# Performance work log

Measured on AMD Instinct MI355X. Metric: run time of the kernel, lower is better.

Reference implementation:

```python
import jax, jax.numpy as jnp
import numpy as np

B, S, H, NH = 2, 2048, 1024, 16
HD = H // NH  # head dim = 64


def setup_inputs() -> dict:
    key = jax.random.key(0)
    ks = jax.random.split(key, 11)
    s = 1.0 / np.sqrt(H)
    return {
        "q": jax.random.normal(ks[0], (B, S, H), jnp.float32),
        "k": jax.random.normal(ks[1], (B, S, H), jnp.float32),
        "v": jax.random.normal(ks[2], (B, S, H), jnp.float32),
        "Wq": jax.random.normal(ks[3], (H, H), jnp.float32) * s,
        "bq": jax.random.normal(ks[4], (H,), jnp.float32) * 0.02,
        "Wk": jax.random.normal(ks[5], (H, H), jnp.float32) * s,
        "bk": jax.random.normal(ks[6], (H,), jnp.float32) * 0.02,
        "Wv": jax.random.normal(ks[7], (H, H), jnp.float32) * s,
        "bv": jax.random.normal(ks[8], (H,), jnp.float32) * 0.02,
        "Wo": jax.random.normal(ks[9], (H, H), jnp.float32) * s,
        "bo": jax.random.normal(ks[10], (H,), jnp.float32) * 0.02,
    }


def reference(q, k, v, Wq, bq, Wk, bk, Wv, bv, Wo, bo):
    # QKV projections: [B,S,H]
    qp = q @ Wq + bq
    kp = k @ Wk + bk
    vp = v @ Wv + bv
    # split heads -> [B, NH, S, HD]
    def split(x):
        return x.reshape(B, S, NH, HD).transpose(0, 2, 1, 3)
    qh, kh, vh = split(qp), split(kp), split(vp)
    # scores [B, NH, S, S], scale by sqrt(head_dim)
    scores = jnp.einsum('bhqd,bhkd->bhqk', qh, kh) / jnp.sqrt(jnp.asarray(HD, qh.dtype))
    attn = jax.nn.softmax(scores, axis=-1)  # attention_dropout p=0.0 (eval)
    ctx = jnp.einsum('bhqk,bhkd->bhqd', attn, vh)
    # merge heads -> [B, S, H]
    ctx = ctx.transpose(0, 2, 1, 3).reshape(B, S, H)
    out = ctx @ Wo + bo  # dropout p=0.0 (eval)
    return out
```

## Files before the change

kernel.cpp:

```cpp
#include <hip/hip_runtime.h>

typedef unsigned short u16;
typedef __attribute__((ext_vector_type(8))) short bf16x8;
typedef __attribute__((ext_vector_type(4))) float f32x4;
typedef __attribute__((ext_vector_type(4))) unsigned short u16x4;

#define B_  2
#define S_  2048
#define H_  1024
#define NH_ 16
#define HD_ 64
#define MR_ (B_*S_)
#define K_  H_

__device__ __forceinline__ u16 f2bf(float f) {
  union { float f; unsigned u; } x; x.f = f;
  unsigned r = x.u + 0x7fffu + ((x.u >> 16) & 1u);
  return (u16)(r >> 16);
}

__device__ __forceinline__ unsigned cvtpk(float lo, float hi) {
  unsigned r;
  asm("v_cvt_pk_bf16_f32 %0, %1, %2" : "=v"(r) : "v"(lo), "v"(hi));
  return r;
}

__device__ __forceinline__ void gload16(const u16* g, u16* l) {
  __builtin_amdgcn_global_load_lds((const __attribute__((address_space(1))) void*)g,
                                   (__attribute__((address_space(3))) void*)l, 16, 0, 0);
}

__global__ __launch_bounds__(256) void cvt3(const float* __restrict__ q, const float* __restrict__ k,
                                            const float* __restrict__ v, u16* __restrict__ dst) {
  const float* src = blockIdx.z == 0 ? q : blockIdx.z == 1 ? k : v;
  u16* d = dst + (size_t)blockIdx.z * MR_ * H_;
  size_t i = ((size_t)blockIdx.x * 256 + threadIdx.x) * 4;
  float4 f = *(const float4*)(src + i);
  u16x4 o = { f2bf(f.x), f2bf(f.y), f2bf(f.z), f2bf(f.w) };
  *(u16x4*)(d + i) = o;
}

__global__ __launch_bounds__(256) void wtrans(const float* __restrict__ Wq, const float* __restrict__ Wk,
                                              const float* __restrict__ Wv, const float* __restrict__ Wo,
                                              u16* __restrict__ wt) {
  const int z = blockIdx.z;
  const float* W = z == 0 ? Wq : z == 1 ? Wk : z == 2 ? Wv : Wo;
  u16* Wt = wt + (size_t)z * H_ * K_;
  __shared__ float t[32][33];
  const int n0 = blockIdx.x * 32, k0 = blockIdx.y * 32;
  const int tx = threadIdx.x & 31, ty = threadIdx.x >> 5;
  #pragma unroll
  for (int i = 0; i < 4; i++) t[ty + 8*i][tx] = W[(size_t)(k0 + ty + 8*i) * H_ + n0 + tx];
  __syncthreads();
  #pragma unroll
  for (int i = 0; i < 4; i++) Wt[(size_t)(n0 + ty + 8*i) * K_ + k0 + tx] = f2bf(t[tx][ty + 8*i]);
}

template <int MODE>
__device__ __forceinline__ void gemm_body(const u16* __restrict__ A, const u16* __restrict__ Bt,
                                          const float* __restrict__ bias, float scale,
                                          u16* __restrict__ Obf, float* __restrict__ Of,
                                          int m_tile, int n_tile) {
  __shared__ u16 ldsA[128 * 64];
  __shared__ u16 ldsB[128 * 64];
  const int tid = threadIdx.x;
  const int lane = tid & 63, wave = tid >> 6;
  const int wm = wave >> 1, wn = wave & 1;
  const int m0 = m_tile * 128, n0 = n_tile * 128;

  f32x4 acc[4][4] = {};

  const int srow = tid >> 3;
  const int sslot = (tid & 7) ^ (srow & 7);
  const u16* ga = A + (size_t)(m0 + srow) * K_ + sslot * 8;
  const u16* gb = Bt + (size_t)(n0 + srow) * K_ + sslot * 8;
  u16* la = ldsA + tid * 8;
  u16* lb = ldsB + tid * 8;

  const int fr = lane & 15;
  const int kg = lane >> 4;

  for (int k0 = 0; k0 < K_; k0 += 64) {
    #pragma unroll
    for (int j = 0; j < 4; j++) gload16(ga + (size_t)(j * 32) * K_ + k0, la + j * 2048);
    #pragma unroll
    for (int j = 0; j < 4; j++) gload16(gb + (size_t)(j * 32) * K_ + k0, lb + j * 2048);
    __syncthreads();

    #pragma unroll
    for (int kk = 0; kk < 2; kk++) {
      const int ps = (((kk << 2) | kg) ^ (fr & 7)) * 8;
      bf16x8 a[4], b[4];
      #pragma unroll
      for (int mf = 0; mf < 4; mf++)
        a[mf] = *(const bf16x8*)&ldsA[(wm * 64 + mf * 16 + fr) * 64 + ps];
      #pragma unroll
      for (int nf = 0; nf < 4; nf++)
        b[nf] = *(const bf16x8*)&ldsB[(wn * 64 + nf * 16 + fr) * 64 + ps];
      #pragma unroll
      for (int mf = 0; mf < 4; mf++)
        #pragma unroll
        for (int nf = 0; nf < 4; nf++)
          acc[mf][nf] = __builtin_amdgcn_mfma_f32_16x16x32_bf16(a[mf], b[nf], acc[mf][nf], 0, 0, 0);
    }
    __syncthreads();
  }

  float bcol[4];
  #pragma unroll
  for (int nf = 0; nf < 4; nf++) bcol[nf] = bias[n0 + wn * 64 + nf * 16 + fr];

  if (MODE == 2) {
    #pragma unroll
    for (int mf = 0; mf < 4; mf++) {
      const int row0 = m0 + wm * 64 + mf * 16 + kg * 4;
      #pragma unroll
      for (int nf = 0; nf < 4; nf++) {
        const int col = n0 + wn * 64 + nf * 16 + fr;
        u16x4 o;
        #pragma unroll
        for (int r = 0; r < 4; r++) o[r] = f2bf(acc[mf][nf][r] + bcol[nf]);
        size_t idx = (((size_t)(col + ((row0 >> 11) << 10))) << 11) + (row0 & 2047);
        *(u16x4*)(Obf + idx) = o;
      }
    }
  } else {
    #pragma unroll
    for (int mf = 0; mf < 4; mf++)
      #pragma unroll
      for (int r = 0; r < 4; r++) {
        const int row = m0 + wm * 64 + mf * 16 + kg * 4 + r;
        #pragma unroll
        for (int nf = 0; nf < 4; nf++) {
          const int col = n0 + wn * 64 + nf * 16 + fr;
          float val = (acc[mf][nf][r] + bcol[nf]) * scale;
          if (MODE == 0) Obf[(size_t)row * H_ + col] = f2bf(val);
          else           Of [(size_t)row * H_ + col] = val;
        }
      }
  }
}

__global__ __launch_bounds__(256) void gemm_qkv(const u16* __restrict__ xb, const u16* __restrict__ wt,
                                                const float* __restrict__ b0, const float* __restrict__ b1,
                                                const float* __restrict__ b2,
                                                u16* __restrict__ QKo, u16* __restrict__ VTo) {
  const int z = blockIdx.z;
  const u16* A = xb + (size_t)z * MR_ * K_;
  const u16* Bt = wt + (size_t)z * H_ * K_;
  if (z == 2) {
    gemm_body<2>(A, Bt, b2, 1.0f, VTo, nullptr, blockIdx.y, blockIdx.x);
  } else {
    const float* bias = z == 0 ? b0 : b1;
    const float scale = z == 0 ? 0.18033688011112042f : 1.0f;
    gemm_body<0>(A, Bt, bias, scale, QKo + (size_t)z * MR_ * H_, nullptr, blockIdx.y, blockIdx.x);
  }
}

__global__ __launch_bounds__(256) void gemm_out(const u16* __restrict__ ctx, const u16* __restrict__ wot,
                                                const float* __restrict__ bo, float* __restrict__ out) {
  gemm_body<1>(ctx, wot, bo, 1.0f, nullptr, out, blockIdx.y, blockIdx.x);
}

__global__ __launch_bounds__(256) void attn(const u16* __restrict__ qp, const u16* __restrict__ kp,
                                            const u16* __restrict__ vt, u16* __restrict__ ctx) {
  __shared__ u16 Kl[2][64 * 64];
  __shared__ u16 Vl[2][64 * 64];
  __shared__ u16 Plds[4][16 * 64];
  const int bh = blockIdx.y;
  const int b = bh >> 4, h = bh & 15;
  const int q0 = blockIdx.x * 64;
  const int tid = threadIdx.x;
  const int wave = tid >> 6, lane = tid & 63;
  const int fr = lane & 15, kg = lane >> 4;

  const u16* Q   = qp + (size_t)b * S_ * H_ + h * HD_;
  const u16* Kb  = kp + (size_t)b * S_ * H_ + h * HD_;
  const u16* Vtb = vt + (size_t)bh * HD_ * S_;
  u16* O = ctx + (size_t)b * S_ * H_ + h * HD_;
  u16* Pw = Plds[wave];

  const int srow = tid >> 3;
  const int sslot = (tid & 7) ^ (srow & 7);

  const int qrow = q0 + wave * 16 + fr;
  bf16x8 qf[2];
  qf[0] = *(const bf16x8*)&Q[(size_t)qrow * H_ + kg * 8];
  qf[1] = *(const bf16x8*)&Q[(size_t)qrow * H_ + 32 + kg * 8];

  f32x4 oacc[4] = {};
  float m_run = -1e30f, l_run = 0.f;

  #pragma unroll
  for (int j = 0; j < 2; j++) {
    gload16(Kb + (size_t)(srow + 32 * j) * H_ + sslot * 8, &Kl[0][0] + j * 2048 + tid * 8);
    gload16(Vtb + (size_t)(srow + 32 * j) * S_ + sslot * 8, &Vl[0][0] + j * 2048 + tid * 8);
  }

  for (int it = 0; it < S_ / 64; ++it) {
    const int s0 = it * 64, cur = it & 1;
    __syncthreads();
    if (it + 1 < S_ / 64) {
      #pragma unroll
      for (int j = 0; j < 2; j++) {
        gload16(Kb + (size_t)(s0 + 64 + srow + 32 * j) * H_ + sslot * 8,
                &Kl[cur ^ 1][0] + j * 2048 + tid * 8);
        gload16(Vtb + (size_t)(srow + 32 * j) * S_ + s0 + 64 + sslot * 8,
                &Vl[cur ^ 1][0] + j * 2048 + tid * 8);
      }
    }
    f32x4 sc[4] = {};
    __builtin_amdgcn_s_setprio(1);
    #pragma unroll
    for (int cf = 0; cf < 4; cf++) {
      const int s = cf * 16 + fr;
      #pragma unroll
      for (int kk = 0; kk < 2; kk++) {
        bf16x8 kf = *(const bf16x8*)&Kl[cur][s * 64 + ((((kk << 2) | kg) ^ (fr & 7)) << 3)];
        sc[cf] = __builtin_amdgcn_mfma_f32_16x16x32_bf16(kf, qf[kk], sc[cf], 0, 0, 0);
      }
    }
    __builtin_amdgcn_s_setprio(0);
    float m4[4];
    #pragma unroll
    for (int r = 0; r < 4; r++)
      m4[r] = fmaxf(fmaxf(sc[0][r], sc[1][r]), fmaxf(sc[2][r], sc[3][r]));
    float tmax = fmaxf(fmaxf(m4[0], m4[1]), fmaxf(m4[2], m4[3]));
    tmax = fmaxf(tmax, __shfl_xor(tmax, 16, 64));
    tmax = fmaxf(tmax, __shfl_xor(tmax, 32, 64));
    if (!__all(tmax <= m_run + 8.0f)) {
      const float mn = fmaxf(m_run, tmax);
      const float sf = __builtin_amdgcn_exp2f(m_run - mn);
      m_run = mn;
      float sfq[4];
      const int lbase = lane & 48;
      #pragma unroll
      for (int r = 0; r < 4; r++) sfq[r] = __shfl(sf, lbase | (kg * 4 + r), 64);
      #pragma unroll
      for (int nf = 0; nf < 4; nf++)
        #pragma unroll
        for (int r = 0; r < 4; r++) oacc[nf][r] *= sfq[r];
      l_run *= sf;
    }
    float psum = 0.f;
    #pragma unroll
    for (int cf = 0; cf < 4; cf++) {
      #pragma unroll
      for (int r = 0; r < 4; r++) { sc[cf][r] = __builtin_amdgcn_exp2f(sc[cf][r] - m_run); psum += sc[cf][r]; }
      uint2 o = { cvtpk(sc[cf][0], sc[cf][1]), cvtpk(sc[cf][2], sc[cf][3]) };
      const int slot = cf * 2 + (kg >> 1);
      *(uint2*)&Pw[fr * 64 + ((slot ^ (fr & 7)) << 3) + ((kg & 1) << 2)] = o;
    }
    psum += __shfl_xor(psum, 16, 64);
    psum += __shfl_xor(psum, 32, 64);
    l_run += psum;
    __builtin_amdgcn_s_setprio(1);
    #pragma unroll
    for (int kk = 0; kk < 2; kk++) {
      bf16x8 pf = *(const bf16x8*)&Pw[fr * 64 + ((((kk << 2) | kg) ^ (fr & 7)) << 3)];
      #pragma unroll
      for (int nf = 0; nf < 4; nf++) {
        const int d = nf * 16 + fr;
        bf16x8 vf = *(const bf16x8*)&Vl[cur][d * 64 + ((((kk << 2) | kg) ^ (d & 7)) << 3)];
        oacc[nf] = __builtin_amdgcn_mfma_f32_16x16x32_bf16(pf, vf, oacc[nf], 0, 0, 0);
      }
    }
    __builtin_amdgcn_s_setprio(0);
  }
  float lq[4];
  const int lbase = lane & 48;
  #pragma unroll
  for (int r = 0; r < 4; r++) lq[r] = 1.0f / __shfl(l_run, lbase | (kg * 4 + r), 64);
  #pragma unroll
  for (int nf = 0; nf < 4; nf++)
    #pragma unroll
    for (int r = 0; r < 4; r++) {
      int row = q0 + wave * 16 + kg * 4 + r;
      O[(size_t)row * H_ + nf * 16 + fr] = f2bf(oacc[nf][r] * lq[r]);
    }
}

extern "C" void kernel_launch(void* const* d_in, const int* in_sizes, int n_in,
                              void* d_out, int out_size, void* d_ws, size_t ws_size,
                              hipStream_t stream) {
  const float* q  = (const float*)d_in[0];
  const float* k  = (const float*)d_in[1];
  const float* v  = (const float*)d_in[2];
  const float* Wq = (const float*)d_in[3];
  const float* bq = (const float*)d_in[4];
  const float* Wk = (const float*)d_in[5];
  const float* bk = (const float*)d_in[6];
  const float* Wv = (const float*)d_in[7];
  const float* bv = (const float*)d_in[8];
  const float* Wo = (const float*)d_in[9];
  const float* bo = (const float*)d_in[10];
  float* out = (float*)d_out;

  char* ws = (char*)d_ws;
  const size_t MB = 1024 * 1024;
  u16* xb   = (u16*)(ws);
  u16* wt   = (u16*)(ws + 24 * MB);
  u16* qkp  = (u16*)(ws + 32 * MB);
  u16* vtp  = (u16*)(ws + 48 * MB);
  u16* ctx  = (u16*)(ws);

  cvt3  <<<dim3(4096, 1, 3), 256, 0, stream>>>(q, k, v, xb);
  wtrans<<<dim3(32, 32, 4),  256, 0, stream>>>(Wq, Wk, Wv, Wo, wt);
  gemm_qkv<<<dim3(8, 32, 3), 256, 0, stream>>>(xb, wt, bq, bk, bv, qkp, vtp);
  attn  <<<dim3(32, 32),     256, 0, stream>>>(qkp, qkp + (size_t)MR_ * H_, vtp, ctx);
  gemm_out<<<dim3(8, 32, 1), 256, 0, stream>>>(ctx, wt + (size_t)3 * H_ * K_, bo, out);
}
```

Baseline: 156.7 us.

## Switch attention to 32x32x16 MFMA with register-resident P and 128-row query tiles

The attention kernel now uses 32x32x16 bf16 MFMAs, with each wave owning 32 query rows, so a block covers 128 queries and the grid is halved. Each K/V tile loaded into LDS is therefore reused across twice as many queries. The S^T output layout lets the row max and sum reduce with a single cross-half shuffle. P is rebuilt as the A operand through register shuffles instead of an LDS round trip. In exchange, register pressure rises from the 16-wide accumulators, and only 512 blocks launch, which may underfill the CUs.

```diff
diff --git a/kernel.cpp b/kernel.cpp
--- a/kernel.cpp
+++ b/kernel.cpp
@@ -3,7 +3,9 @@
 typedef unsigned short u16;
 typedef __attribute__((ext_vector_type(8))) short bf16x8;
 typedef __attribute__((ext_vector_type(4))) float f32x4;
+typedef __attribute__((ext_vector_type(16))) float f32x16;
 typedef __attribute__((ext_vector_type(4))) unsigned short u16x4;
+typedef __attribute__((ext_vector_type(4))) unsigned int u32x4;
 
 #define B_  2
 #define S_  2048
@@ -166,29 +168,28 @@
                                             const u16* __restrict__ vt, u16* __restrict__ ctx) {
   __shared__ u16 Kl[2][64 * 64];
   __shared__ u16 Vl[2][64 * 64];
-  __shared__ u16 Plds[4][16 * 64];
   const int bh = blockIdx.y;
   const int b = bh >> 4, h = bh & 15;
-  const int q0 = blockIdx.x * 64;
+  const int q0 = blockIdx.x * 128;
   const int tid = threadIdx.x;
-  const int wave = tid >> 6, lane = tid & 63;
-  const int fr = lane & 15, kg = lane >> 4;
+  const int w = tid >> 6, l = tid & 63;
+  const int ql = l & 31, hi = l >> 5;
 
   const u16* Q   = qp + (size_t)b * S_ * H_ + h * HD_;
   const u16* Kb  = kp + (size_t)b * S_ * H_ + h * HD_;
   const u16* Vtb = vt + (size_t)bh * HD_ * S_;
   u16* O = ctx + (size_t)b * S_ * H_ + h * HD_;
-  u16* Pw = Plds[wave];
 
   const int srow = tid >> 3;
   const int sslot = (tid & 7) ^ (srow & 7);
 
-  const int qrow = q0 + wave * 16 + fr;
-  bf16x8 qf[2];
-  qf[0] = *(const bf16x8*)&Q[(size_t)qrow * H_ + kg * 8];
-  qf[1] = *(const bf16x8*)&Q[(size_t)qrow * H_ + 32 + kg * 8];
-
-  f32x4 oacc[4] = {};
+  const int qrow = q0 + w * 32 + ql;
+  bf16x8 qf[4];
+  #pragma unroll
+  for (int ds = 0; ds < 4; ds++)
+    qf[ds] = *(const bf16x8*)&Q[(size_t)qrow * H_ + ds * 16 + hi * 8];
+
+  f32x16 oacc0 = {}, oacc1 = {};
   float m_run = -1e30f, l_run = 0.f;
 
   #pragma unroll
@@ -209,75 +210,93 @@
                 &Vl[cur ^ 1][0] + j * 2048 + tid * 8);
       }
     }
-    f32x4 sc[4] = {};
+    f32x16 sc0 = {}, sc1 = {};
     __builtin_amdgcn_s_setprio(1);
     #pragma unroll
-    for (int cf = 0; cf < 4; cf++) {
-      const int s = cf * 16 + fr;
-      #pragma unroll
-      for (int kk = 0; kk < 2; kk++) {
-        bf16x8 kf = *(const bf16x8*)&Kl[cur][s * 64 + ((((kk << 2) | kg) ^ (fr & 7)) << 3)];
-        sc[cf] = __builtin_amdgcn_mfma_f32_16x16x32_bf16(kf, qf[kk], sc[cf], 0, 0, 0);
-      }
+    for (int ds = 0; ds < 4; ds++) {
+      const int sl = ((ds * 2 + hi) ^ (ql & 7)) << 3;
+      bf16x8 k0 = *(const bf16x8*)&Kl[cur][ql * 64 + sl];
+      bf16x8 k1 = *(const bf16x8*)&Kl[cur][(32 + ql) * 64 + sl];
+      sc0 = __builtin_amdgcn_mfma_f32_32x32x16_bf16(k0, qf[ds], sc0, 0, 0, 0);
+      sc1 = __builtin_amdgcn_mfma_f32_32x32x16_bf16(k1, qf[ds], sc1, 0, 0, 0);
     }
     __builtin_amdgcn_s_setprio(0);
-    float m4[4];
-    #pragma unroll
-    for (int r = 0; r < 4; r++)
-      m4[r] = fmaxf(fmaxf(sc[0][r], sc[1][r]), fmaxf(sc[2][r], sc[3][r]));
-    float tmax = fmaxf(fmaxf(m4[0], m4[1]), fmaxf(m4[2], m4[3]));
-    tmax = fmaxf(tmax, __shfl_xor(tmax, 16, 64));
+    float t4[8];
+    #pragma unroll
+    for (int g = 0; g < 4; g++) {
+      t4[g]     = fmaxf(fmaxf(sc0[4*g], sc0[4*g+1]), fmaxf(sc0[4*g+2], sc0[4*g+3]));
+      t4[4 + g] = fmaxf(fmaxf(sc1[4*g], sc1[4*g+1]), fmaxf(sc1[4*g+2], sc1[4*g+3]));
+    }
+    float tmax = fmaxf(fmaxf(fmaxf(t4[0], t4[1]), fmaxf(t4[2], t4[3])),
+                       fmaxf(fmaxf(t4[4], t4[5]), fmaxf(t4[6], t4[7])));
     tmax = fmaxf(tmax, __shfl_xor(tmax, 32, 64));
     if (!__all(tmax <= m_run + 8.0f)) {
       const float mn = fmaxf(m_run, tmax);
       const float sf = __builtin_amdgcn_exp2f(m_run - mn);
       m_run = mn;
-      float sfq[4];
-      const int lbase = lane & 48;
-      #pragma unroll
-      for (int r = 0; r < 4; r++) sfq[r] = __shfl(sf, lbase | (kg * 4 + r), 64);
-      #pragma unroll
-      for (int nf = 0; nf < 4; nf++)
-        #pragma unroll
-        for (int r = 0; r < 4; r++) oacc[nf][r] *= sfq[r];
       l_run *= sf;
-    }
-    float psum = 0.f;
-    #pragma unroll
-    for (int cf = 0; cf < 4; cf++) {
-      #pragma unroll
-      for (int r = 0; r < 4; r++) { sc[cf][r] = __builtin_amdgcn_exp2f(sc[cf][r] - m_run); psum += sc[cf][r]; }
-      uint2 o = { cvtpk(sc[cf][0], sc[cf][1]), cvtpk(sc[cf][2], sc[cf][3]) };
-      const int slot = cf * 2 + (kg >> 1);
-      *(uint2*)&Pw[fr * 64 + ((slot ^ (fr & 7)) << 3) + ((kg & 1) << 2)] = o;
-    }
-    psum += __shfl_xor(psum, 16, 64);
+      #pragma unroll
+      for (int r = 0; r < 16; r++) {
+        const float sfq = __shfl(sf, (r & 3) + 8 * (r >> 2) + 4 * hi, 64);
+        oacc0[r] *= sfq;
+        oacc1[r] *= sfq;
+      }
+    }
+    float ps4[8];
+    #pragma unroll
+    for (int g = 0; g < 4; g++) {
+      #pragma unroll
+      for (int m = 0; m < 4; m++) {
+        sc0[4*g+m] = __builtin_amdgcn_exp2f(sc0[4*g+m] - m_run);
+        sc1[4*g+m] = __builtin_amdgcn_exp2f(sc1[4*g+m] - m_run);
+      }
+      ps4[g]     = (sc0[4*g] + sc0[4*g+1]) + (sc0[4*g+2] + sc0[4*g+3]);
+      ps4[4 + g] = (sc1[4*g] + sc1[4*g+1]) + (sc1[4*g+2] + sc1[4*g+3]);
+    }
+    float psum = ((ps4[0] + ps4[1]) + (ps4[2] + ps4[3])) + ((ps4[4] + ps4[5]) + (ps4[6] + ps4[7]));
     psum += __shfl_xor(psum, 32, 64);
     l_run += psum;
+    uint2 pk0[4], pk1[4];
+    #pragma unroll
+    for (int g = 0; g < 4; g++) {
+      pk0[g].x = cvtpk(sc0[4*g], sc0[4*g+1]);  pk0[g].y = cvtpk(sc0[4*g+2], sc0[4*g+3]);
+      pk1[g].x = cvtpk(sc1[4*g], sc1[4*g+1]);  pk1[g].y = cvtpk(sc1[4*g+2], sc1[4*g+3]);
+    }
     __builtin_amdgcn_s_setprio(1);
     #pragma unroll
-    for (int kk = 0; kk < 2; kk++) {
-      bf16x8 pf = *(const bf16x8*)&Pw[fr * 64 + ((((kk << 2) | kg) ^ (fr & 7)) << 3)];
-      #pragma unroll
-      for (int nf = 0; nf < 4; nf++) {
-        const int d = nf * 16 + fr;
-        bf16x8 vf = *(const bf16x8*)&Vl[cur][d * 64 + ((((kk << 2) | kg) ^ (d & 7)) << 3)];
-        oacc[nf] = __builtin_amdgcn_mfma_f32_16x16x32_bf16(pf, vf, oacc[nf], 0, 0, 0);
+    for (int ks = 0; ks < 4; ks++) {
+      const int gb = (ks & 1) * 2;
+      const uint2 pa = (ks < 2) ? pk0[gb]     : pk1[gb];
+      const uint2 pb = (ks < 2) ? pk0[gb + 1] : pk1[gb + 1];
+      uint2 own, snd;
+      own.x = hi ? pb.x : pa.x;  own.y = hi ? pb.y : pa.y;
+      snd.x = hi ? pa.x : pb.x;  snd.y = hi ? pa.y : pb.y;
+      uint2 rcv;
+      rcv.x = __shfl_xor((int)snd.x, 32, 64);
+      rcv.y = __shfl_xor((int)snd.y, 32, 64);
+      u32x4 fu;
+      fu.x = hi ? rcv.x : own.x;  fu.y = hi ? rcv.y : own.y;
+      fu.z = hi ? own.x : rcv.x;  fu.w = hi ? own.y : rcv.y;
+      const bf16x8 pfrag = __builtin_bit_cast(bf16x8, fu);
+      #pragma unroll
+      for (int dt = 0; dt < 2; dt++) {
+        const int d = dt * 32 + ql;
+        bf16x8 vf = *(const bf16x8*)&Vl[cur][d * 64 + (((ks * 2 + hi) ^ (d & 7)) << 3)];
+        if (dt == 0) oacc0 = __builtin_amdgcn_mfma_f32_32x32x16_bf16(pfrag, vf, oacc0, 0, 0, 0);
+        else         oacc1 = __builtin_amdgcn_mfma_f32_32x32x16_bf16(pfrag, vf, oacc1, 0, 0, 0);
       }
     }
     __builtin_amdgcn_s_setprio(0);
   }
-  float lq[4];
-  const int lbase = lane & 48;
-  #pragma unroll
-  for (int r = 0; r < 4; r++) lq[r] = 1.0f / __shfl(l_run, lbase | (kg * 4 + r), 64);
-  #pragma unroll
-  for (int nf = 0; nf < 4; nf++)
-    #pragma unroll
-    for (int r = 0; r < 4; r++) {
-      int row = q0 + wave * 16 + kg * 4 + r;
-      O[(size_t)row * H_ + nf * 16 + fr] = f2bf(oacc[nf][r] * lq[r]);
-    }
+  const float linv = 1.0f / l_run;
+  #pragma unroll
+  for (int r = 0; r < 16; r++) {
+    const int qi = (r & 3) + 8 * (r >> 2) + 4 * hi;
+    const float lq = __shfl(linv, qi, 64);
+    const int row = q0 + w * 32 + qi;
+    O[(size_t)row * H_ + ql]      = f2bf(oacc0[r] * lq);
+    O[(size_t)row * H_ + 32 + ql] = f2bf(oacc1[r] * lq);
+  }
 }
 
 extern "C" void kernel_launch(void* const* d_in, const int* in_sizes, int n_in,
@@ -307,6 +326,6 @@
   cvt3  <<<dim3(4096, 1, 3), 256, 0, stream>>>(q, k, v, xb);
   wtrans<<<dim3(32, 32, 4),  256, 0, stream>>>(Wq, Wk, Wv, Wo, wt);
   gemm_qkv<<<dim3(8, 32, 3), 256, 0, stream>>>(xb, wt, bq, bk, bv, qkp, vtp);
-  attn  <<<dim3(32, 32),     256, 0, stream>>>(qkp, qkp + (size_t)MR_ * H_, vtp, ctx);
+  attn  <<<dim3(16, 32),     256, 0, stream>>>(qkp, qkp + (size_t)MR_ * H_, vtp, ctx);
   gemm_out<<<dim3(8, 32, 1), 256, 0, stream>>>(ctx, wt + (size_t)3 * H_ * K_, bo, out);
 }
```

Result: faster. 153.6 us (-2.0%).
